# Kernel optimization log

Hardware: AMD Instinct MI355X
Metric: run time of the kernel (lower is better)

The kernel has to match this reference:

```python
import jax, jax.numpy as jnp
import numpy as np
import math

B, LQ, LK, D = 8, 2048, 2048, 1024  # hidden_dim = O_dim = D


def setup_inputs() -> dict:
    key = jax.random.key(0)
    ks = jax.random.split(key, 9)
    s = 1.0 / math.sqrt(D)
    return {
        "key": jax.random.normal(ks[0], (B, LK, D), dtype=jnp.float32),
        "query": jax.random.normal(ks[1], (B, LQ, D), dtype=jnp.float32),
        "mask": jax.random.randint(ks[2], (B, LK), 0, 2, dtype=jnp.int32),
        "Wq": jax.random.uniform(ks[3], (D, D), jnp.float32, -s, s),
        "bq": jax.random.uniform(ks[4], (D,), jnp.float32, -s, s),
        "Wk": jax.random.uniform(ks[5], (D, D), jnp.float32, -s, s),
        "bk": jax.random.uniform(ks[6], (D,), jnp.float32, -s, s),
        "Wv": jax.random.uniform(ks[7], (D, D), jnp.float32, -s, s),
        "bv": jax.random.uniform(ks[8], (D,), jnp.float32, -s, s),
    }


def reference(key, query, mask, Wq, bq, Wk, bk, Wv, bv):
    # Linear projections (torch nn.Linear: x @ W.T + b)
    q = jnp.einsum("bld,hd->blh", query, Wq) + bq          # [B, LQ, H]
    k = jnp.einsum("bld,hd->blh", key, Wk) + bk            # [B, LK, H]
    # Quirk of original module: values Linear is applied to the PROJECTED key
    v = jnp.einsum("blh,oh->blo", k, Wv) + bv              # [B, LK, O]
    score = jnp.einsum("bqh,bkh->bqk", q, k) / math.sqrt(D)
    # mask_score: mask [B, LK] -> [B, 1, LK], fill zeros with -1e9
    score = jnp.where(mask[:, None, :] == 0, jnp.float32(-1e9), score)
    score = jax.nn.softmax(score, axis=-1)
    # dropout in eval mode = identity; NaN cleanup preserved
    score = jnp.where(jnp.isnan(score), jnp.float32(0.0), score)
    output = jnp.einsum("bqk,bko->bqo", score, v)
    return output, score
```

## Files before the change

kernel.cpp:

```cpp
#include <hip/hip_runtime.h>
#include <cstdint>

#define DDIM 1024
#define LQN  2048
#define LKN  2048
#define BBAT 8


typedef short bf16x8 __attribute__((ext_vector_type(8)));
typedef float f32x4  __attribute__((ext_vector_type(4)));

__device__ __forceinline__ unsigned short f2bf(float f) {
    union { float f; unsigned int i; } x; x.f = f;
    unsigned int r = (x.i + 0x7fffu + ((x.i >> 16) & 1u)) >> 16;
    return (unsigned short)r;
}
__device__ __forceinline__ bf16x8 cvt8(const float* p) {
    float4 x0 = *(const float4*)p;
    float4 x1 = *(const float4*)(p + 4);
    bf16x8 r;
    r[0] = (short)f2bf(x0.x); r[1] = (short)f2bf(x0.y);
    r[2] = (short)f2bf(x0.z); r[3] = (short)f2bf(x0.w);
    r[4] = (short)f2bf(x1.x); r[5] = (short)f2bf(x1.y);
    r[6] = (short)f2bf(x1.z); r[7] = (short)f2bf(x1.w);
    return r;
}

__device__ __forceinline__ void gl2lds16(const void* g, void* l) {
    __builtin_amdgcn_global_load_lds(
        reinterpret_cast<const __attribute__((address_space(1))) void*>(
            reinterpret_cast<uintptr_t>(g)),
        reinterpret_cast<__attribute__((address_space(3))) void*>(
            (unsigned)reinterpret_cast<uintptr_t>(l)),
        16, 0, 0);
}

__global__ __launch_bounds__(256)
void cast_bf16(const float* __restrict__ in, unsigned short* __restrict__ out,
               long n8)
{
    long i = (long)blockIdx.x * blockDim.x + threadIdx.x;
    const long stride = (long)gridDim.x * blockDim.x;
    for (; i < n8; i += stride)
        *(bf16x8*)(out + i * 8) = cvt8(in + i * 8);
}

template<int MODE>
__global__ __launch_bounds__(256)
void gemm_nt(const unsigned short* __restrict__ A,
             const unsigned short* __restrict__ B,
             const float* __restrict__ bias,
             const int* __restrict__ mask,
             void* __restrict__ out)
{
    constexpr int K   = (MODE == 3) ? LKN : DDIM;
    constexpr int LDA = K;
    constexpr int LDB = K;
    constexpr int NT  = K / 32;

    __shared__ unsigned short lds[2][8192];

    const int t    = threadIdx.x;
    const int lane = t & 63;
    const int wave = t >> 6;
    const int wm   = wave >> 1;
    const int wn   = wave & 1;

    const int gx   = gridDim.x;
    const int nwg  = gx * gridDim.y;
    const int bid0 = blockIdx.y * gx + blockIdx.x;
    const int bid  = ((nwg & 7) == 0) ? ((bid0 & 7) * (nwg >> 3) + (bid0 >> 3))
                                      : bid0;
    const int bm = bid / gx;
    const int bn = bid % gx;
    const int z  = blockIdx.z;

    const unsigned short* Ap = A;
    const unsigned short* Bp = B;
    if (MODE == 2) { Ap += (long)z * LQN * DDIM; Bp += (long)z * LKN * DDIM; }
    if (MODE == 3) { Ap += (long)z * LQN * LKN;  Bp += (long)z * DDIM * LKN; }

    const int srow = t >> 2;
    const int skk  = (t & 3) * 8;
    const unsigned short* ga0 = Ap + (long)(bm * 128 + srow) * LDA + skk;
    const unsigned short* ga1 = ga0 + 64L * LDA;
    const unsigned short* gb0 = Bp + (long)(bn * 128 + srow) * LDB + skk;
    const unsigned short* gb1 = gb0 + 64L * LDB;
    const int woff = wave * 512;

    f32x4 acc[4][4];
    #pragma unroll
    for (int i = 0; i < 4; ++i)
        #pragma unroll
        for (int j = 0; j < 4; ++j)
            acc[i][j] = (f32x4)(0.0f);

    const int quad = lane >> 4;
    const int l15  = lane & 15;

#define STAGE(bufp, kk) do {                              \
        gl2lds16(ga0 + (kk), (bufp) + woff);              \
        gl2lds16(ga1 + (kk), (bufp) + woff + 2048);       \
        gl2lds16(gb0 + (kk), (bufp) + 4096 + woff);       \
        gl2lds16(gb1 + (kk), (bufp) + 4096 + woff + 2048);\
    } while (0)

    unsigned short* cur = &lds[0][0];
    unsigned short* nxt = &lds[1][0];

    STAGE(cur, 0);
    __syncthreads();

    for (int tt = 0; tt < NT; ++tt) {
        if (tt + 1 < NT)
            STAGE(nxt, (tt + 1) * 32);

        bf16x8 af[4], bfv[4];
        #pragma unroll
        for (int i = 0; i < 4; ++i)
            af[i] = *(const bf16x8*)&cur[(wm * 64 + i * 16 + l15) * 32 + quad * 8];
        #pragma unroll
        for (int j = 0; j < 4; ++j)
            bfv[j] = *(const bf16x8*)&cur[4096 + (wn * 64 + j * 16 + l15) * 32 + quad * 8];

        #pragma unroll
        for (int i = 0; i < 4; ++i)
            #pragma unroll
            for (int j = 0; j < 4; ++j)
                acc[i][j] = __builtin_amdgcn_mfma_f32_16x16x32_bf16(
                    af[i], bfv[j], acc[i][j], 0, 0, 0);

        __syncthreads();
        unsigned short* tmp = cur; cur = nxt; nxt = tmp;
    }
#undef STAGE

    #pragma unroll
    for (int i = 0; i < 4; ++i) {
        #pragma unroll
        for (int j = 0; j < 4; ++j) {
            const int grow = bm * 128 + wm * 64 + i * 16 + quad * 4;
            const int gcol = bn * 128 + wn * 64 + j * 16 + l15;
            if (MODE == 0) {
                const float bc = bias[gcol];
                #pragma unroll
                for (int r = 0; r < 4; ++r)
                    ((unsigned short*)out)[(long)(grow + r) * DDIM + gcol] =
                        f2bf(acc[i][j][r] + bc);
            } else if (MODE == 1) {
                const int b2 = gcol >> 11;
                const int lk = gcol & 2047;
                #pragma unroll
                for (int r = 0; r < 4; ++r) {
                    const float bc = bias[grow + r];
                    ((unsigned short*)out)[(long)b2 * DDIM * LKN +
                                           (long)(grow + r) * LKN + lk] =
                        f2bf(acc[i][j][r] + bc);
                }
            } else if (MODE == 2) {
                const int mv = mask[z * LKN + gcol];
                #pragma unroll
                for (int r = 0; r < 4; ++r) {
                    float v = acc[i][j][r] * 0.03125f;
                    if (mv == 0) v = -1e9f;
                    ((float*)out)[(long)z * LQN * LKN +
                                  (long)(grow + r) * LKN + gcol] = v;
                }
            } else {
                #pragma unroll
                for (int r = 0; r < 4; ++r)
                    ((float*)out)[(long)z * LQN * DDIM +
                                  (long)(grow + r) * DDIM + gcol] = acc[i][j][r];
            }
        }
    }
}

__global__ __launch_bounds__(256)
void softmax_rows(float* __restrict__ P, unsigned short* __restrict__ Pb)
{
    const int t = threadIdx.x;
    const long base = (long)blockIdx.x * LKN + t * 8;

    float4 r0 = *(const float4*)&P[base];
    float4 r1 = *(const float4*)&P[base + 4];
    float v[8] = { r0.x, r0.y, r0.z, r0.w, r1.x, r1.y, r1.z, r1.w };

    float m = -3.0e38f;
    #pragma unroll
    for (int i = 0; i < 8; ++i) m = fmaxf(m, v[i]);
    #pragma unroll
    for (int off = 32; off >= 1; off >>= 1) m = fmaxf(m, __shfl_xor(m, off, 64));
    __shared__ float redm[4];
    if ((t & 63) == 0) redm[t >> 6] = m;
    __syncthreads();
    m = fmaxf(fmaxf(redm[0], redm[1]), fmaxf(redm[2], redm[3]));

    float s = 0.0f;
    #pragma unroll
    for (int i = 0; i < 8; ++i) { v[i] = __expf(v[i] - m); s += v[i]; }
    #pragma unroll
    for (int off = 32; off >= 1; off >>= 1) s += __shfl_xor(s, off, 64);
    __shared__ float reds[4];
    if ((t & 63) == 0) reds[t >> 6] = s;
    __syncthreads();
    s = reds[0] + reds[1] + reds[2] + reds[3];

    const float inv = 1.0f / s;
    r0.x = v[0] * inv; r0.y = v[1] * inv; r0.z = v[2] * inv; r0.w = v[3] * inv;
    r1.x = v[4] * inv; r1.y = v[5] * inv; r1.z = v[6] * inv; r1.w = v[7] * inv;
    *(float4*)&P[base]     = r0;
    *(float4*)&P[base + 4] = r1;

    bf16x8 pb;
    pb[0] = (short)f2bf(r0.x); pb[1] = (short)f2bf(r0.y);
    pb[2] = (short)f2bf(r0.z); pb[3] = (short)f2bf(r0.w);
    pb[4] = (short)f2bf(r1.x); pb[5] = (short)f2bf(r1.y);
    pb[6] = (short)f2bf(r1.z); pb[7] = (short)f2bf(r1.w);
    *(bf16x8*)&Pb[base] = pb;
}

extern "C" void kernel_launch(void* const* d_in, const int* in_sizes, int n_in,
                              void* d_out, int out_size, void* d_ws, size_t ws_size,
                              hipStream_t stream)
{
    (void)in_sizes; (void)n_in; (void)out_size;

    const float* key   = (const float*)d_in[0];
    const float* query = (const float*)d_in[1];
    const int*   mask  = (const int*)d_in[2];
    const float* Wq    = (const float*)d_in[3];
    const float* bq    = (const float*)d_in[4];
    const float* Wk    = (const float*)d_in[5];
    const float* bk    = (const float*)d_in[6];
    const float* Wv    = (const float*)d_in[7];
    const float* bv    = (const float*)d_in[8];

    float* outO = (float*)d_out;
    float* outP = outO + (size_t)BBAT * LQN * DDIM;

    unsigned short* Wqb  = (unsigned short*)d_ws;
    unsigned short* Wkb  = Wqb + (size_t)DDIM * DDIM;
    unsigned short* Wvb  = Wkb + (size_t)DDIM * DDIM;
    unsigned short* gbuf = Wvb + (size_t)DDIM * DDIM;

    const size_t fixed = (size_t)3 * DDIM * DDIM * sizeof(unsigned short);
    const size_t perB  = ((size_t)LQN * LKN + (size_t)3 * LQN * DDIM) *
                         sizeof(unsigned short);
    size_t avail = (ws_size > fixed) ? (ws_size - fixed) : 0;
    int g = (int)(avail / perB);
    if (g > BBAT) g = BBAT;
    if (g < 1)    g = 1;

    dim3 blk(256, 1, 1);

    cast_bf16<<<dim3(512, 1, 1), blk, 0, stream>>>(Wq, Wqb, (long)DDIM * DDIM / 8);
    cast_bf16<<<dim3(512, 1, 1), blk, 0, stream>>>(Wk, Wkb, (long)DDIM * DDIM / 8);
    cast_bf16<<<dim3(512, 1, 1), blk, 0, stream>>>(Wv, Wvb, (long)DDIM * DDIM / 8);

    for (int b0 = 0; b0 < BBAT; b0 += g) {
        const int gl = (BBAT - b0 < g) ? (BBAT - b0) : g;

        unsigned short* regionA = gbuf;
        unsigned short* qc = regionA;
        unsigned short* kc = regionA + (size_t)gl * LQN * DDIM;
        unsigned short* Pb = regionA;
        unsigned short* Qp = regionA + (size_t)gl * LQN * LKN;
        unsigned short* Kp = Qp + (size_t)gl * LQN * DDIM;
        unsigned short* Vt = Kp + (size_t)gl * LKN * DDIM;

        cast_bf16<<<dim3(2048, 1, 1), blk, 0, stream>>>(
            query + (size_t)b0 * LQN * DDIM, qc, (long)gl * LQN * DDIM / 8);
        cast_bf16<<<dim3(2048, 1, 1), blk, 0, stream>>>(
            key + (size_t)b0 * LKN * DDIM, kc, (long)gl * LKN * DDIM / 8);

        gemm_nt<0><<<dim3(8, gl * 16, 1), blk, 0, stream>>>(qc, Wqb, bq, nullptr, Qp);

        gemm_nt<0><<<dim3(8, gl * 16, 1), blk, 0, stream>>>(kc, Wkb, bk, nullptr, Kp);

        gemm_nt<1><<<dim3(gl * 16, 8, 1), blk, 0, stream>>>(Wvb, Kp, bv, nullptr, Vt);

        gemm_nt<2><<<dim3(16, 16, gl), blk, 0, stream>>>(
            Qp, Kp, nullptr, mask + (size_t)b0 * LKN,
            outP + (size_t)b0 * LQN * LKN);

        softmax_rows<<<dim3(gl * LQN, 1, 1), blk, 0, stream>>>(
            outP + (size_t)b0 * LQN * LKN, Pb);

        gemm_nt<3><<<dim3(8, 16, gl), blk, 0, stream>>>(
            Pb, Vt, nullptr, nullptr, outO + (size_t)b0 * LQN * DDIM);
    }
}
```

Baseline: 721.0 us.

## Enlarge GEMM tiles to 256x256 with 8 waves and triple-buffered async LDS pipeline

All GEMM stages switch from a 128x128 tile with 4 waves to a 256x256 tile with 8 waves (512 threads). Each wave now computes 128x64. Loads become a 3-stage ring of LDS buffers fed by direct global-to-LDS copies, synchronised with explicit vmcnt waits and raw barriers in place of __syncthreads, and s_setprio is raised around the MFMA block. The goal is more data reuse per byte loaded and better overlap of memory traffic with compute. The cost is 96KB of LDS and many more accumulator registers per thread, which lowers occupancy, and fewer workgroups per launch, which can leave compute units underfilled.

```diff
diff --git a/kernel.cpp b/kernel.cpp
--- a/kernel.cpp
+++ b/kernel.cpp
@@ -46,7 +46,7 @@
 }
 
 template<int MODE>
-__global__ __launch_bounds__(256)
+__global__ __launch_bounds__(512)
 void gemm_nt(const unsigned short* __restrict__ A,
              const unsigned short* __restrict__ B,
              const float* __restrict__ bias,
@@ -58,13 +58,13 @@
     constexpr int LDB = K;
     constexpr int NT  = K / 32;
 
-    __shared__ unsigned short lds[2][8192];
+    __shared__ unsigned short lds[3 * 16384];
 
     const int t    = threadIdx.x;
     const int lane = t & 63;
     const int wave = t >> 6;
-    const int wm   = wave >> 1;
-    const int wn   = wave & 1;
+    const int wm   = wave >> 2;
+    const int wn   = wave & 3;
 
     const int gx   = gridDim.x;
     const int nwg  = gx * gridDim.y;
@@ -82,15 +82,15 @@
 
     const int srow = t >> 2;
     const int skk  = (t & 3) * 8;
-    const unsigned short* ga0 = Ap + (long)(bm * 128 + srow) * LDA + skk;
-    const unsigned short* ga1 = ga0 + 64L * LDA;
-    const unsigned short* gb0 = Bp + (long)(bn * 128 + srow) * LDB + skk;
-    const unsigned short* gb1 = gb0 + 64L * LDB;
+    const unsigned short* ga0 = Ap + (long)(bm * 256 + srow) * LDA + skk;
+    const unsigned short* ga1 = ga0 + 128L * LDA;
+    const unsigned short* gb0 = Bp + (long)(bn * 256 + srow) * LDB + skk;
+    const unsigned short* gb1 = gb0 + 128L * LDB;
     const int woff = wave * 512;
 
-    f32x4 acc[4][4];
-    #pragma unroll
-    for (int i = 0; i < 4; ++i)
+    f32x4 acc[8][4];
+    #pragma unroll
+    for (int i = 0; i < 8; ++i)
         #pragma unroll
         for (int j = 0; j < 4; ++j)
             acc[i][j] = (f32x4)(0.0f);
@@ -98,49 +98,57 @@
     const int quad = lane >> 4;
     const int l15  = lane & 15;
 
-#define STAGE(bufp, kk) do {                              \
-        gl2lds16(ga0 + (kk), (bufp) + woff);              \
-        gl2lds16(ga1 + (kk), (bufp) + woff + 2048);       \
-        gl2lds16(gb0 + (kk), (bufp) + 4096 + woff);       \
-        gl2lds16(gb1 + (kk), (bufp) + 4096 + woff + 2048);\
+#define STAGE(bi, kt) do {                                              \
+        unsigned short* sb = &lds[(bi) * 16384];                        \
+        const int ko = (kt) * 32;                                       \
+        gl2lds16(ga0 + ko, sb + woff);                                  \
+        gl2lds16(ga1 + ko, sb + 4096  + woff);                          \
+        gl2lds16(gb0 + ko, sb + 8192  + woff);                          \
+        gl2lds16(gb1 + ko, sb + 12288 + woff);                          \
     } while (0)
 
-    unsigned short* cur = &lds[0][0];
-    unsigned short* nxt = &lds[1][0];
-
-    STAGE(cur, 0);
-    __syncthreads();
-
+    STAGE(0, 0);
+    STAGE(1, 1);
+    asm volatile("s_waitcnt vmcnt(4)" ::: "memory");
+    __builtin_amdgcn_s_barrier();
+
+    int cb = 0;
     for (int tt = 0; tt < NT; ++tt) {
-        if (tt + 1 < NT)
-            STAGE(nxt, (tt + 1) * 32);
-
-        bf16x8 af[4], bfv[4];
-        #pragma unroll
-        for (int i = 0; i < 4; ++i)
-            af[i] = *(const bf16x8*)&cur[(wm * 64 + i * 16 + l15) * 32 + quad * 8];
+        const int nb = (cb + 2 >= 3) ? (cb - 1) : (cb + 2);
+        const bool st = (tt + 2 < NT);
+        if (st) STAGE(nb, tt + 2);
+
+        const unsigned short* sb = &lds[cb * 16384];
+        bf16x8 af[8], bfv[4];
         #pragma unroll
         for (int j = 0; j < 4; ++j)
-            bfv[j] = *(const bf16x8*)&cur[4096 + (wn * 64 + j * 16 + l15) * 32 + quad * 8];
-
-        #pragma unroll
-        for (int i = 0; i < 4; ++i)
+            bfv[j] = *(const bf16x8*)&sb[8192 + (wn * 64 + j * 16 + l15) * 32 + quad * 8];
+        #pragma unroll
+        for (int i = 0; i < 8; ++i)
+            af[i] = *(const bf16x8*)&sb[(wm * 128 + i * 16 + l15) * 32 + quad * 8];
+
+        __builtin_amdgcn_s_setprio(1);
+        #pragma unroll
+        for (int i = 0; i < 8; ++i)
             #pragma unroll
             for (int j = 0; j < 4; ++j)
                 acc[i][j] = __builtin_amdgcn_mfma_f32_16x16x32_bf16(
                     af[i], bfv[j], acc[i][j], 0, 0, 0);
-
-        __syncthreads();
-        unsigned short* tmp = cur; cur = nxt; nxt = tmp;
+        __builtin_amdgcn_s_setprio(0);
+
+        if (st) asm volatile("s_waitcnt vmcnt(4)" ::: "memory");
+        else    asm volatile("s_waitcnt vmcnt(0)" ::: "memory");
+        __builtin_amdgcn_s_barrier();
+        cb = (cb + 1 >= 3) ? 0 : (cb + 1);
     }
 #undef STAGE
 
     #pragma unroll
-    for (int i = 0; i < 4; ++i) {
+    for (int i = 0; i < 8; ++i) {
         #pragma unroll
         for (int j = 0; j < 4; ++j) {
-            const int grow = bm * 128 + wm * 64 + i * 16 + quad * 4;
-            const int gcol = bn * 128 + wn * 64 + j * 16 + l15;
+            const int grow = bm * 256 + wm * 128 + i * 16 + quad * 4;
+            const int gcol = bn * 256 + wn * 64 + j * 16 + l15;
             if (MODE == 0) {
                 const float bc = bias[gcol];
                 #pragma unroll
@@ -253,6 +261,7 @@
     if (g < 1)    g = 1;
 
     dim3 blk(256, 1, 1);
+    dim3 gblk(512, 1, 1);
 
     cast_bf16<<<dim3(512, 1, 1), blk, 0, stream>>>(Wq, Wqb, (long)DDIM * DDIM / 8);
     cast_bf16<<<dim3(512, 1, 1), blk, 0, stream>>>(Wk, Wkb, (long)DDIM * DDIM / 8);
@@ -274,20 +283,20 @@
         cast_bf16<<<dim3(2048, 1, 1), blk, 0, stream>>>(
             key + (size_t)b0 * LKN * DDIM, kc, (long)gl * LKN * DDIM / 8);
 
-        gemm_nt<0><<<dim3(8, gl * 16, 1), blk, 0, stream>>>(qc, Wqb, bq, nullptr, Qp);
-
-        gemm_nt<0><<<dim3(8, gl * 16, 1), blk, 0, stream>>>(kc, Wkb, bk, nullptr, Kp);
-
-        gemm_nt<1><<<dim3(gl * 16, 8, 1), blk, 0, stream>>>(Wvb, Kp, bv, nullptr, Vt);
-
-        gemm_nt<2><<<dim3(16, 16, gl), blk, 0, stream>>>(
+        gemm_nt<0><<<dim3(4, gl * 8, 1), gblk, 0, stream>>>(qc, Wqb, bq, nullptr, Qp);
+
+        gemm_nt<0><<<dim3(4, gl * 8, 1), gblk, 0, stream>>>(kc, Wkb, bk, nullptr, Kp);
+
+        gemm_nt<1><<<dim3(gl * 8, 4, 1), gblk, 0, stream>>>(Wvb, Kp, bv, nullptr, Vt);
+
+        gemm_nt<2><<<dim3(8, 8, gl), gblk, 0, stream>>>(
             Qp, Kp, nullptr, mask + (size_t)b0 * LKN,
             outP + (size_t)b0 * LQN * LKN);
 
         softmax_rows<<<dim3(gl * LQN, 1, 1), blk, 0, stream>>>(
             outP + (size_t)b0 * LQN * LKN, Pb);
 
-        gemm_nt<3><<<dim3(8, 16, gl), blk, 0, stream>>>(
+        gemm_nt<3><<<dim3(4, 8, gl), gblk, 0, stream>>>(
             Pb, Vt, nullptr, nullptr, outO + (size_t)b0 * LQN * DDIM);
     }
 }
```

After: 623.1 us. 13.6% less time.
